# Optimization experiments

Hardware: AMD Instinct MI355X
Metric: run time of the kernel (lower is better)

## Reference

```python
import jax, jax.numpy as jnp
import numpy as np

B, T, D, H = 16, 512, 1024, 16
HD = D // H  # 64
EPS = 1e-5


def _ln(x, g, b):
    m = x.mean(-1, keepdims=True)
    v = ((x - m) ** 2).mean(-1, keepdims=True)
    return (x - m) / jnp.sqrt(v + EPS) * g + b


def setup_inputs() -> dict:
    key = jax.random.key(0)
    ks = jax.random.split(key, 16)
    s = lambda n: 1.0 / np.sqrt(n)
    return {
        "x": jax.random.normal(ks[0], (B, T, D), jnp.float32),
        "ga": jnp.ones((D,), jnp.float32), "ba": jnp.zeros((D,), jnp.float32),
        "Win": jax.random.normal(ks[1], (D, D), jnp.float32) * s(D),
        "bin_": jnp.zeros((D,), jnp.float32),
        "Wk": jax.random.normal(ks[2], (H, D, HD), jnp.float32) * s(D),
        "bk": jnp.zeros((H, HD), jnp.float32),
        "Wq": jax.random.normal(ks[3], (H, D, HD), jnp.float32) * s(D),
        "bq": jnp.zeros((H, HD), jnp.float32),
        "Wv": jax.random.normal(ks[4], (H, D, HD), jnp.float32) * s(D),
        "bv": jnp.zeros((H, HD), jnp.float32),
        "Wout": jax.random.normal(ks[5], (D, D), jnp.float32) * s(D),
        "bout": jnp.zeros((D,), jnp.float32),
        "gf": jnp.ones((D,), jnp.float32), "bf": jnp.zeros((D,), jnp.float32),
        "W1": jax.random.normal(ks[6], (D, 4 * D), jnp.float32) * s(D),
        "b1": jnp.zeros((4 * D,), jnp.float32),
        "W2": jax.random.normal(ks[7], (4 * D, D), jnp.float32) * s(4 * D),
        "b2": jnp.zeros((D,), jnp.float32),
    }


def reference(x, ga, ba, Win, bin_, Wk, bk, Wq, bq, Wv, bv, Wout, bout, gf, bf, W1, b1, W2, b2):
    # --- attention sub-block (pre-norm) ---
    h = _ln(x, ga, ba)
    h = h @ Win + bin_                                   # [B,T,D]
    k = jnp.einsum('btd,hde->bhte', h, Wk) + bk[:, None, :]
    q = jnp.einsum('btd,hde->bhte', h, Wq) + bq[:, None, :]
    v = jnp.einsum('btd,hde->bhte', h, Wv) + bv[:, None, :]
    # NOTE: faithful to source -- scores are K @ Q^T, no 1/sqrt(d) scaling
    wei = jnp.einsum('bhte,bhse->bhts', k, q)            # [B,H,T,T]
    mask = jnp.tril(jnp.ones((T, T), bool))
    wei = jnp.where(mask, wei, -jnp.inf)
    wei = jax.nn.softmax(wei, axis=-1)                   # dropout = eval identity
    o = jnp.einsum('bhts,bhse->bhte', wei, v)            # [B,H,T,HD]
    o = o.transpose(0, 2, 1, 3).reshape(B, T, D)         # concat heads on last dim
    x = o @ Wout + bout + x
    # --- FFN sub-block (pre-norm) ---
    h2 = _ln(x, gf, bf)
    ff = jax.nn.relu(h2 @ W1 + b1) @ W2 + b2
    return ff + x
```

## Files before the change

### kernel.cpp

```cpp
#include <hip/hip_runtime.h>


#define DEV __device__ __forceinline__

typedef unsigned short u16;
typedef __attribute__((ext_vector_type(8))) __bf16 bf16x8;
typedef __attribute__((ext_vector_type(4))) float f32x4;
typedef __attribute__((ext_vector_type(8))) unsigned short u16x8;

typedef __attribute__((address_space(1))) void as1_void;
typedef __attribute__((address_space(3))) void as3_void;

DEV u16 f2b(float f) {
  unsigned u = __float_as_uint(f);
  u = (u + 0x7fffu + ((u >> 16) & 1u)) >> 16;
  return (u16)u;
}
DEV float b2f(u16 h) { return __uint_as_float(((unsigned)h) << 16); }

DEV f32x4 mfma16(bf16x8 a, bf16x8 b, f32x4 c) {
  return __builtin_amdgcn_mfma_f32_16x16x32_bf16(a, b, c, 0, 0, 0);
}

DEV void gload16(const void* g, void* l) {
  __builtin_amdgcn_global_load_lds((as1_void*)(unsigned long long)g,
                                   (as3_void*)(unsigned long long)l,
                                   16u, 0, 0u);
}

#define EPI_BF16 0
#define EPI_RELU 1
#define EPI_RES 2
#define EPI_SPLIT 3
#define EPI_QKFRAG 4
#define EPI_VFRAG 5

template <int BM, int BN, int EPI>
__global__ __launch_bounds__((BM == 256) ? 512 : 256, 2) void gemm256(
    const u16* __restrict__ A, int lda, int kdup, const u16* __restrict__ Bt,
    const float* __restrict__ bias, const float* __restrict__ res,
    void* __restrict__ Cout, void* __restrict__ Cout2, int ldc, int N, int K,
    int ldb, int kdupB) {
  constexpr int THREADS = (BM == 256) ? 512 : 256;
  constexpr int NWAVE = THREADS / 64;
  constexpr int NWN = (BN == 256) ? 4 : 2;
  constexpr int NWM = NWAVE / NWN;
  constexpr int MPW = BM / NWM;
  constexpr int MF = MPW / 16;
  constexpr int LA = BM * 4 / THREADS;
  constexpr int LB = BN * 4 / THREADS;
  constexpr int NWAIT = 2 * (LA + LB);
  constexpr int ASZ = BM * 64;
  constexpr int BSZ = BN * 64;
  constexpr int ATOT = 4 * ASZ;
  __shared__ __align__(1024) char lds[4 * ASZ + 4 * BSZ];

  const int nwg = (int)gridDim.x;
  const int cpx = nwg >> 3;
  int w = (int)blockIdx.x;
  w = (w & 7) * cpx + (w >> 3);
  const int nbn = N / BN;
  const int bn = w % nbn, bm = w / nbn;

  const int tid = threadIdx.x;
  const int wave = tid >> 6, lane = tid & 63;
  const int l15 = lane & 15, l4 = lane >> 4;
  const int wm = wave / NWN;
  const int wn = wave % NWN;
  const int nk = K >> 6;

  const int srow = lane >> 2;
  const int schunk = ((lane & 3) ^ ((srow >> 1) & 3)) << 4;
  const char* Ab = (const char*)A;
  const char* Bb = (const char*)Bt;
  const int arowA = wave * (BM / NWAVE) + srow;
  const int arowB = wave * (BN / NWAVE) + srow;

  auto stageA = [&](int buf, int kh, int kt) {
    const int ktA = (kdup && kt >= kdup) ? kt - kdup : kt;
    const char* s = Ab + (size_t)(bm * BM + arowA) * (size_t)(lda * 2) +
                    ktA * 128 + kh * 64 + schunk;
    char* d = lds + (((buf << 1) | kh) * ASZ) + wave * (LA * 1024);
    gload16(s, d);
    gload16(s + (size_t)16 * (size_t)(lda * 2), d + 1024);
  };
  auto stageB = [&](int buf, int kh, int kt) {
    const int ktB = (kdupB && kt >= kdupB) ? kt - kdupB : kt;
    const char* s = Bb + (size_t)(bn * BN + arowB) * (size_t)(ldb * 2) +
                    ktB * 128 + kh * 64 + schunk;
    char* d = lds + ATOT + (((buf << 1) | kh) * BSZ) + wave * (LB * 1024);
    gload16(s, d);
    if (LB == 2) gload16(s + (size_t)16 * (size_t)(ldb * 2), d + 1024);
  };

  const f32x4 fz = {0.f, 0.f, 0.f, 0.f};
  f32x4 acc[MF][4];
#pragma unroll
  for (int i = 0; i < MF; ++i)
#pragma unroll
    for (int j = 0; j < 4; ++j) acc[i][j] = fz;

  stageA(0, 0, 0);
  stageB(0, 0, 0);
  stageA(0, 1, 0);
  stageB(0, 1, 0);
  {
    const int k1 = (1 < nk) ? 1 : nk - 1;
    stageA(1, 0, k1);
    stageB(1, 0, k1);
  }
  asm volatile("s_waitcnt vmcnt(%0)" ::"i"(NWAIT) : "memory");
  __builtin_amdgcn_s_barrier();

  for (int u = 0; u < nk; ++u) {
    const int cur = u & 1;
    const int kp1 = (u + 1 < nk) ? u + 1 : nk - 1;
    const int kp2 = (u + 2 < nk) ? u + 2 : nk - 1;
#pragma unroll
    for (int kh = 0; kh < 2; ++kh) {
      const char* Ar = lds + (((cur << 1) | kh) * ASZ);
      const char* Br = lds + ATOT + (((cur << 1) | kh) * BSZ);
      bf16x8 bfr[4], af[MF];
#pragma unroll
      for (int ni = 0; ni < 4; ++ni) {
        const int n = wn * 64 + ni * 16 + l15;
        bfr[ni] = *(const bf16x8*)(Br + n * 64 + ((l4 ^ ((n >> 1) & 3)) << 4));
      }
#pragma unroll
      for (int mi = 0; mi < MF; ++mi) {
        const int m = wm * MPW + mi * 16 + l15;
        af[mi] = *(const bf16x8*)(Ar + m * 64 + ((l4 ^ ((m >> 1) & 3)) << 4));
      }
      if (kh == 0) {
        stageA(cur ^ 1, 1, kp1);
        stageB(cur ^ 1, 1, kp1);
      } else {
        stageA(cur, 0, kp2);
        stageB(cur, 0, kp2);
      }
      __builtin_amdgcn_s_setprio(1);
#pragma unroll
      for (int mi = 0; mi < MF; ++mi)
#pragma unroll
        for (int ni = 0; ni < 4; ++ni)
          acc[mi][ni] = mfma16(af[mi], bfr[ni], acc[mi][ni]);
      __builtin_amdgcn_s_setprio(0);
      asm volatile("s_waitcnt lgkmcnt(0)" ::: "memory");
      asm volatile("s_waitcnt vmcnt(%0)" ::"i"(NWAIT) : "memory");
      __builtin_amdgcn_s_barrier();
    }
  }
  asm volatile("s_waitcnt vmcnt(0)" ::: "memory");

#pragma unroll
  for (int mf = 0; mf < MF; ++mf) {
#pragma unroll
    for (int ni = 0; ni < 4; ++ni) {
      const int gn = bn * BN + wn * 64 + ni * 16 + l15;
      const float bia = bias[gn];
#pragma unroll
      for (int r = 0; r < 4; ++r) {
        const int gm = bm * BM + wm * MPW + mf * 16 + l4 * 4 + r;
        float v = acc[mf][ni][r] + bia;
        if (EPI == EPI_BF16) {
          ((u16*)Cout)[(size_t)gm * ldc + gn] = f2b(v);
        } else if (EPI == EPI_RELU) {
          ((u16*)Cout)[(size_t)gm * ldc + gn] = f2b(v > 0.f ? v : 0.f);
        } else if (EPI == EPI_RES) {
          ((float*)Cout)[(size_t)gm * ldc + gn] =
              v + res[(size_t)gm * ldc + gn];
        } else if (EPI == EPI_SPLIT) {
          u16 hi = f2b(v);
          ((u16*)Cout)[(size_t)gm * ldc + gn] = hi;
          ((u16*)Cout)[(size_t)gm * ldc + N + gn] = f2b(v - b2f(hi));
        } else if (EPI == EPI_QKFRAG) {
          const int b = gm >> 9, s = gm & 511;
          const int gs = s >> 4, sr = s & 15;
          const int n = gn & 1023;
          const int h = n >> 6, e = n & 63;
          u16* base = (u16*)((gn >> 10) ? Cout2 : Cout);
          const size_t blk = ((size_t)(b * 16 + h) * 32 + gs) * 4;
          const int idx = ((e >> 3) & 3) * 128 + sr * 8 + (e & 7);
          const u16 hi = f2b(v);
          base[(blk + (e >> 5)) * 512 + idx] = hi;
          base[(blk + 2 + (e >> 5)) * 512 + idx] = f2b(v - b2f(hi));
        } else {
          const int b = gm >> 9, s = gm & 511;
          const int h = gn >> 6, e = gn & 63;
          const size_t blk =
              ((size_t)(b * 16 + h) * 16 + (s >> 5)) * 4 + (e >> 4);
          ((u16*)Cout)[blk * 512 + ((s >> 3) & 3) * 128 + (e & 15) * 8 +
                       (s & 7)] = f2b(v);
        }
      }
    }
  }
}

template <bool SPLIT>
__global__ __launch_bounds__(256) void lnorm(const float* __restrict__ x,
                                             const float* __restrict__ g,
                                             const float* __restrict__ bt,
                                             u16* __restrict__ out) {
  const int row = blockIdx.x, tid = threadIdx.x;
  const int wave = tid >> 6, lane = tid & 63;
  const float4 v = *(const float4*)(x + (size_t)row * 1024 + tid * 4);
  float xv[4] = {v.x, v.y, v.z, v.w};
  float s = xv[0] + xv[1] + xv[2] + xv[3];
  float s2 = xv[0] * xv[0] + xv[1] * xv[1] + xv[2] * xv[2] + xv[3] * xv[3];
  for (int off = 32; off; off >>= 1) {
    s += __shfl_down(s, off);
    s2 += __shfl_down(s2, off);
  }
  __shared__ float red[8];
  if (lane == 0) {
    red[wave] = s;
    red[4 + wave] = s2;
  }
  __syncthreads();
  const float ts = red[0] + red[1] + red[2] + red[3];
  const float ts2 = red[4] + red[5] + red[6] + red[7];
  const float mean = ts * (1.f / 1024.f);
  const float var = ts2 * (1.f / 1024.f) - mean * mean;
  const float rstd = rsqrtf(var + 1e-5f);
#pragma unroll
  for (int j = 0; j < 4; ++j) {
    const int col = tid * 4 + j;
    const float y = (xv[j] - mean) * rstd * g[col] + bt[col];
    const u16 hi = f2b(y);
    if (SPLIT) {
      out[(size_t)row * 2048 + col] = hi;
      out[(size_t)row * 2048 + 1024 + col] = f2b(y - b2f(hi));
    } else {
      out[(size_t)row * 1024 + col] = hi;
    }
  }
}

template <int MODE>
__global__ __launch_bounds__(256) void wtrans(const float* __restrict__ in,
                                              int kstride, long ibs,
                                              u16* __restrict__ out, int ors,
                                              long obs, int Koff) {
  in += (size_t)blockIdx.z * ibs;
  out += (size_t)blockIdx.z * obs;
  const int n0 = blockIdx.x * 64, k0 = blockIdx.y * 64;
  const int tid = threadIdx.x;
  __shared__ float tt[64][65];
  const int r = tid >> 4, c4 = (tid & 15) * 4;
#pragma unroll
  for (int p = 0; p < 4; ++p) {
    const int rr = r + p * 16;
    const float4 vv =
        *(const float4*)(in + (size_t)(k0 + rr) * kstride + n0 + c4);
    tt[rr][c4] = vv.x;
    tt[rr][c4 + 1] = vv.y;
    tt[rr][c4 + 2] = vv.z;
    tt[rr][c4 + 3] = vv.w;
  }
  __syncthreads();
  const int nl = tid >> 2, kc = (tid & 3) * 16;
  u16 hi[16], lo[16];
#pragma unroll
  for (int j = 0; j < 16; ++j) {
    const float w2 = tt[kc + j][nl];
    hi[j] = f2b(w2);
    if (MODE == 2) lo[j] = f2b(w2 - b2f(hi[j]));
  }
  u16* orow = out + (size_t)(n0 + nl) * ors + k0 + kc;
  u16x8 a, b;
#pragma unroll
  for (int j = 0; j < 8; ++j) {
    a[j] = hi[j];
    b[j] = hi[8 + j];
  }
  *(u16x8*)(orow) = a;
  *(u16x8*)(orow + 8) = b;
  if (MODE == 2) {
    *(u16x8*)(orow + 2 * Koff) = a;
    *(u16x8*)(orow + 2 * Koff + 8) = b;
    u16x8 c, d;
#pragma unroll
    for (int j = 0; j < 8; ++j) {
      c[j] = lo[j];
      d[j] = lo[8 + j];
    }
    *(u16x8*)(orow + Koff) = c;
    *(u16x8*)(orow + Koff + 8) = d;
  }
}

__global__ void biascat(const float* __restrict__ bq,
                        const float* __restrict__ bk, float* __restrict__ o) {
  const int i = blockIdx.x * 256 + threadIdx.x;
  o[i] = (i < 1024) ? bq[i] : bk[i - 1024];
}

__global__ void fillconst(float* __restrict__ p, float v, int n) {
  const int i = blockIdx.x * 256 + threadIdx.x;
  if (i < n) p[i] = v;
}

__global__ __launch_bounds__(256) void attn_fwd(const u16* __restrict__ qf,
                                                const u16* __restrict__ kf,
                                                const u16* __restrict__ vf,
                                                u16* __restrict__ o) {
  const int bh = blockIdx.y;
  const int b = bh >> 4, h = bh & 15;
  const int tid = threadIdx.x, wave = tid >> 6, lane = tid & 63;
  const int l15 = lane & 15, l4 = lane >> 4;
  const int g0 = (int)blockIdx.x * 4 + wave;
  __shared__ u16 Pl[4][1024];

  const f32x4 fz = {0.f, 0.f, 0.f, 0.f};
  const u16* qfb = qf + (size_t)bh * 32 * 2048 + lane * 8;
  const u16* vfb = vf + (size_t)bh * 16 * 2048 + lane * 8;

  for (int grp = 0; grp < 2; ++grp) {
    const int gt = grp ? (31 - g0) : g0;
    const int tw = gt * 16;
    const u16* kfb = kf + ((size_t)(bh * 32 + gt) * 4) * 512 + lane * 8;
    const bf16x8 kh0 = *(const bf16x8*)(kfb);
    const bf16x8 kh1 = *(const bf16x8*)(kfb + 512);
    const bf16x8 kl0 = *(const bf16x8*)(kfb + 1024);
    const bf16x8 kl1 = *(const bf16x8*)(kfb + 1536);

    f32x4 oacc[4] = {fz, fz, fz, fz};
    float mrow[4] = {-1e30f, -1e30f, -1e30f, -1e30f};
    float lrow[4] = {0.f, 0.f, 0.f, 0.f};
    const int niter = (tw + 79) >> 6;

    for (int it = 0; it < niter; ++it) {
      const int s0 = it * 64;
      bf16x8 qh[4][2], ql[4][2];
#pragma unroll
      for (int scb = 0; scb < 4; ++scb) {
        const u16* qp = qfb + (size_t)((s0 >> 4) + scb) * 2048;
        qh[scb][0] = *(const bf16x8*)(qp);
        qh[scb][1] = *(const bf16x8*)(qp + 512);
        ql[scb][0] = *(const bf16x8*)(qp + 1024);
        ql[scb][1] = *(const bf16x8*)(qp + 1536);
      }
      bf16x8 vv[2][4];
#pragma unroll
      for (int h2 = 0; h2 < 2; ++h2) {
        const u16* vp = vfb + (size_t)((s0 >> 5) + h2) * 2048;
#pragma unroll
        for (int eF = 0; eF < 4; ++eF)
          vv[h2][eF] = *(const bf16x8*)(vp + eF * 512);
      }
      f32x4 sf[4];
#pragma unroll
      for (int scb = 0; scb < 4; ++scb) {
        f32x4 z = fz;
        z = mfma16(kh0, qh[scb][0], z);
        z = mfma16(kh1, qh[scb][1], z);
        z = mfma16(kh0, ql[scb][0], z);
        z = mfma16(kh1, ql[scb][1], z);
        z = mfma16(kl0, qh[scb][0], z);
        z = mfma16(kl1, qh[scb][1], z);
        sf[scb] = z;
      }
      if (s0 + 63 > tw) {
#pragma unroll
        for (int scb = 0; scb < 4; ++scb)
#pragma unroll
          for (int r = 0; r < 4; ++r) {
            const int s = s0 + scb * 16 + l15, t = tw + l4 * 4 + r;
            if (s > t) sf[scb][r] = -1e30f;
          }
      }
      float scl[4];
#pragma unroll
      for (int r = 0; r < 4; ++r) {
        float v = fmaxf(fmaxf(sf[0][r], sf[1][r]), fmaxf(sf[2][r], sf[3][r]));
        v = fmaxf(v, __shfl_xor(v, 1));
        v = fmaxf(v, __shfl_xor(v, 2));
        v = fmaxf(v, __shfl_xor(v, 4));
        v = fmaxf(v, __shfl_xor(v, 8));
        const float mn = fmaxf(mrow[r], v);
        scl[r] = __expf(mrow[r] - mn);
        mrow[r] = mn;
      }
      float ps[4] = {0.f, 0.f, 0.f, 0.f};
#pragma unroll
      for (int scb = 0; scb < 4; ++scb)
#pragma unroll
        for (int r = 0; r < 4; ++r) {
          const float p = __expf(sf[scb][r] - mrow[r]);
          sf[scb][r] = p;
          ps[r] += p;
        }
#pragma unroll
      for (int r = 0; r < 4; ++r) {
        float v = ps[r];
        v += __shfl_xor(v, 1);
        v += __shfl_xor(v, 2);
        v += __shfl_xor(v, 4);
        v += __shfl_xor(v, 8);
        lrow[r] = lrow[r] * scl[r] + v;
        oacc[0][r] *= scl[r];
        oacc[1][r] *= scl[r];
        oacc[2][r] *= scl[r];
        oacc[3][r] *= scl[r];
      }
#pragma unroll
      for (int scb = 0; scb < 4; ++scb)
#pragma unroll
        for (int r = 0; r < 4; ++r) {
          const int trow = l4 * 4 + r, scol = scb * 16 + l15;
          const int byte = trow * 128 + ((scol * 2) ^ ((trow & 7) << 4));
          *(u16*)((char*)&Pl[wave][0] + byte) = f2b(sf[scb][r]);
        }
#pragma unroll
      for (int h2 = 0; h2 < 2; ++h2) {
        const bf16x8 pf = *(const bf16x8*)((const char*)&Pl[wave][0] +
                                           l15 * 128 +
                                           (((h2 * 4 + l4) ^ (l15 & 7)) << 4));
#pragma unroll
        for (int eF = 0; eF < 4; ++eF)
          oacc[eF] = mfma16(pf, vv[h2][eF], oacc[eF]);
      }
    }
#pragma unroll
    for (int eF = 0; eF < 4; ++eF)
#pragma unroll
      for (int r = 0; r < 4; ++r) {
        const int t = tw + l4 * 4 + r;
        const float val = oacc[eF][r] / lrow[r];
        o[(size_t)(b * 512 + t) * 1024 + h * 64 + eF * 16 + l15] = f2b(val);
      }
  }
}

extern "C" void kernel_launch(void* const* d_in, const int* in_sizes, int n_in,
                              void* d_out, int out_size, void* d_ws,
                              size_t ws_size, hipStream_t stream) {
  const float* x = (const float*)d_in[0];
  const float* ga = (const float*)d_in[1];
  const float* ba = (const float*)d_in[2];
  const float* Win = (const float*)d_in[3];
  const float* bin = (const float*)d_in[4];
  const float* Wk = (const float*)d_in[5];
  const float* bk = (const float*)d_in[6];
  const float* Wq = (const float*)d_in[7];
  const float* bq = (const float*)d_in[8];
  const float* Wv = (const float*)d_in[9];
  const float* bv = (const float*)d_in[10];
  const float* Wout = (const float*)d_in[11];
  const float* bout = (const float*)d_in[12];
  const float* gf = (const float*)d_in[13];
  const float* bf_ = (const float*)d_in[14];
  const float* W1 = (const float*)d_in[15];
  const float* b1 = (const float*)d_in[16];
  const float* W2 = (const float*)d_in[17];
  const float* b2 = (const float*)d_in[18];
  float* out = (float*)d_out;

  char* ws = (char*)d_ws;
  size_t off = 0;
  auto alloc = [&](size_t bytes) {
    char* p = ws + off;
    off += (bytes + 255) & ~(size_t)255;
    return p;
  };
  u16* WinT = (u16*)alloc((size_t)1024 * 1024 * 2);
  u16* WqkT = (u16*)alloc((size_t)2048 * 1024 * 2);
  u16* WvT = (u16*)alloc((size_t)1024 * 1024 * 2);
  u16* WoutT = (u16*)alloc((size_t)1024 * 1024 * 2);
  u16* W1T = (u16*)alloc((size_t)4096 * 1024 * 2);
  u16* W2T = (u16*)alloc((size_t)1024 * 4096 * 2);
  float* bqk = (float*)alloc(2048 * 4);
  char* R1 = alloc((size_t)8192 * 2048 * 2);
  char* R2 = alloc((size_t)8192 * 2048 * 2);
  char* QK = alloc((size_t)2 * 256 * 32 * 4 * 1024);
  const size_t need = off;

  if (need > ws_size) {
    fillconst<<<(out_size + 255) / 256, 256, 0, stream>>>(out, 12345.0f,
                                                          out_size);
    return;
  }

  u16* ln1 = (u16*)R1;
  u16* vfb = (u16*)R1;
  u16* hb = (u16*)R2;
  u16* ob = (u16*)R2;
  u16* ln2 = (u16*)(R2 + (size_t)8192 * 1024 * 2);
  u16* qfb = (u16*)QK;
  u16* kfb = (u16*)(QK + (size_t)256 * 32 * 4 * 1024);
  u16* ffn1 = (u16*)QK;
  float* x2 = out;

  wtrans<0><<<dim3(16, 16, 1), 256, 0, stream>>>(Win, 1024, 0, WinT, 1024, 0,
                                                 0);
  wtrans<0><<<dim3(1, 16, 16), 256, 0, stream>>>(Wq, 64, 65536, WqkT, 1024,
                                                 (long)64 * 1024, 0);
  wtrans<0><<<dim3(1, 16, 16), 256, 0, stream>>>(
      Wk, 64, 65536, WqkT + (size_t)1024 * 1024, 1024, (long)64 * 1024, 0);
  wtrans<0><<<dim3(1, 16, 16), 256, 0, stream>>>(Wv, 64, 65536, WvT, 1024,
                                                 (long)64 * 1024, 0);
  wtrans<0><<<dim3(16, 16, 1), 256, 0, stream>>>(Wout, 1024, 0, WoutT, 1024, 0,
                                                 0);
  wtrans<0><<<dim3(64, 16, 1), 256, 0, stream>>>(W1, 4096, 0, W1T, 1024, 0, 0);
  wtrans<0><<<dim3(16, 64, 1), 256, 0, stream>>>(W2, 1024, 0, W2T, 4096, 0, 0);
  biascat<<<8, 256, 0, stream>>>(bq, bk, bqk);

  lnorm<true><<<8192, 256, 0, stream>>>(x, ga, ba, ln1);
  gemm256<256, 128, EPI_BF16><<<256, 512, 0, stream>>>(
      ln1, 2048, 0, WinT, bin, nullptr, hb, nullptr, 1024, 1024, 2048, 1024,
      16);
  gemm256<256, 256, EPI_QKFRAG><<<256, 512, 0, stream>>>(
      hb, 1024, 0, WqkT, bqk, nullptr, qfb, kfb, 0, 2048, 1024, 1024, 0);
  gemm256<256, 128, EPI_VFRAG><<<256, 512, 0, stream>>>(
      hb, 1024, 0, WvT, bv, nullptr, vfb, nullptr, 0, 1024, 1024, 1024, 0);
  attn_fwd<<<dim3(4, 256), 256, 0, stream>>>(qfb, kfb, vfb, ob);
  gemm256<256, 128, EPI_RES><<<256, 512, 0, stream>>>(
      ob, 1024, 0, WoutT, bout, x, x2, nullptr, 1024, 1024, 1024, 1024, 0);
  lnorm<false><<<8192, 256, 0, stream>>>(x2, gf, bf_, ln2);
  gemm256<256, 256, EPI_RELU><<<512, 512, 0, stream>>>(
      ln2, 1024, 0, W1T, b1, nullptr, ffn1, nullptr, 4096, 4096, 1024, 1024,
      0);
  gemm256<256, 128, EPI_RES><<<256, 512, 0, stream>>>(
      ffn1, 4096, 0, W2T, b2, x2, out, nullptr, 1024, 1024, 4096, 4096, 0);
}
```

Baseline: 390.8 us.

## Drop split-precision LN1 input and fuse Q/K/V projections into one GEMM

The first LayerNorm now writes a single bf16 copy, and the input projection GEMM runs over K=1024 instead of 2048, so the hi/lo split-precision trick on that path is gone. The Q, K and V projections are merged into one GEMM with N=3072 and a combined epilogue that writes Q/K fragments (still hi/lo split) and V fragments. This removes one kernel launch and halves the work of the first projection. In exchange, accuracy drops because the LN1 output is rounded to bf16 once.

Measured after the change: 388.7 us. Within noise of the previous version (-0.5%).

```diff
diff --git a/kernel.cpp b/kernel.cpp
--- a/kernel.cpp
+++ b/kernel.cpp
@@ -31,8 +31,7 @@
 #define EPI_BF16 0
 #define EPI_RELU 1
 #define EPI_RES 2
-#define EPI_SPLIT 3
-#define EPI_QKFRAG 4
+#define EPI_QKV 3
 #define EPI_VFRAG 5
 
 template <int BM, int BN, int EPI>
@@ -169,35 +168,32 @@
         } else if (EPI == EPI_RES) {
           ((float*)Cout)[(size_t)gm * ldc + gn] =
               v + res[(size_t)gm * ldc + gn];
-        } else if (EPI == EPI_SPLIT) {
-          u16 hi = f2b(v);
-          ((u16*)Cout)[(size_t)gm * ldc + gn] = hi;
-          ((u16*)Cout)[(size_t)gm * ldc + N + gn] = f2b(v - b2f(hi));
-        } else if (EPI == EPI_QKFRAG) {
+        } else if (EPI == EPI_QKV) {
           const int b = gm >> 9, s = gm & 511;
-          const int gs = s >> 4, sr = s & 15;
-          const int n = gn & 1023;
-          const int h = n >> 6, e = n & 63;
-          u16* base = (u16*)((gn >> 10) ? Cout2 : Cout);
-          const size_t blk = ((size_t)(b * 16 + h) * 32 + gs) * 4;
-          const int idx = ((e >> 3) & 3) * 128 + sr * 8 + (e & 7);
-          const u16 hi = f2b(v);
-          base[(blk + (e >> 5)) * 512 + idx] = hi;
-          base[(blk + 2 + (e >> 5)) * 512 + idx] = f2b(v - b2f(hi));
-        } else {
-          const int b = gm >> 9, s = gm & 511;
-          const int h = gn >> 6, e = gn & 63;
-          const size_t blk =
-              ((size_t)(b * 16 + h) * 16 + (s >> 5)) * 4 + (e >> 4);
-          ((u16*)Cout)[blk * 512 + ((s >> 3) & 3) * 128 + (e & 15) * 8 +
-                       (s & 7)] = f2b(v);
+          if (gn < 2048) {
+            const int gs = s >> 4, sr = s & 15;
+            const int n = gn & 1023;
+            const int h = n >> 6, e = n & 63;
+            u16* base = (u16*)Cout + ((gn >> 10) ? (size_t)16777216 : 0);
+            const size_t blk = ((size_t)(b * 16 + h) * 32 + gs) * 4;
+            const int idx = ((e >> 3) & 3) * 128 + sr * 8 + (e & 7);
+            const u16 hi = f2b(v);
+            base[(blk + (e >> 5)) * 512 + idx] = hi;
+            base[(blk + 2 + (e >> 5)) * 512 + idx] = f2b(v - b2f(hi));
+          } else {
+            const int n = gn - 2048;
+            const int h = n >> 6, e = n & 63;
+            const size_t blk =
+                ((size_t)(b * 16 + h) * 16 + (s >> 5)) * 4 + (e >> 4);
+            ((u16*)Cout2)[blk * 512 + ((s >> 3) & 3) * 128 + (e & 15) * 8 +
+                          (s & 7)] = f2b(v);
+          }
         }
       }
     }
   }
 }
 
-template <bool SPLIT>
 __global__ __launch_bounds__(256) void lnorm(const float* __restrict__ x,
                                              const float* __restrict__ g,
                                              const float* __restrict__ bt,
@@ -227,21 +223,14 @@
   for (int j = 0; j < 4; ++j) {
     const int col = tid * 4 + j;
     const float y = (xv[j] - mean) * rstd * g[col] + bt[col];
-    const u16 hi = f2b(y);
-    if (SPLIT) {
-      out[(size_t)row * 2048 + col] = hi;
-      out[(size_t)row * 2048 + 1024 + col] = f2b(y - b2f(hi));
-    } else {
-      out[(size_t)row * 1024 + col] = hi;
-    }
-  }
-}
-
-template <int MODE>
+    out[(size_t)row * 1024 + col] = f2b(y);
+  }
+}
+
 __global__ __launch_bounds__(256) void wtrans(const float* __restrict__ in,
                                               int kstride, long ibs,
                                               u16* __restrict__ out, int ors,
-                                              long obs, int Koff) {
+                                              long obs) {
   in += (size_t)blockIdx.z * ibs;
   out += (size_t)blockIdx.z * obs;
   const int n0 = blockIdx.x * 64, k0 = blockIdx.y * 64;
@@ -260,40 +249,22 @@
   }
   __syncthreads();
   const int nl = tid >> 2, kc = (tid & 3) * 16;
-  u16 hi[16], lo[16];
-#pragma unroll
-  for (int j = 0; j < 16; ++j) {
-    const float w2 = tt[kc + j][nl];
-    hi[j] = f2b(w2);
-    if (MODE == 2) lo[j] = f2b(w2 - b2f(hi[j]));
+  u16x8 a, b;
+#pragma unroll
+  for (int j = 0; j < 8; ++j) {
+    a[j] = f2b(tt[kc + j][nl]);
+    b[j] = f2b(tt[kc + 8 + j][nl]);
   }
   u16* orow = out + (size_t)(n0 + nl) * ors + k0 + kc;
-  u16x8 a, b;
-#pragma unroll
-  for (int j = 0; j < 8; ++j) {
-    a[j] = hi[j];
-    b[j] = hi[8 + j];
-  }
   *(u16x8*)(orow) = a;
   *(u16x8*)(orow + 8) = b;
-  if (MODE == 2) {
-    *(u16x8*)(orow + 2 * Koff) = a;
-    *(u16x8*)(orow + 2 * Koff + 8) = b;
-    u16x8 c, d;
-#pragma unroll
-    for (int j = 0; j < 8; ++j) {
-      c[j] = lo[j];
-      d[j] = lo[8 + j];
-    }
-    *(u16x8*)(orow + Koff) = c;
-    *(u16x8*)(orow + Koff + 8) = d;
-  }
-}
-
-__global__ void biascat(const float* __restrict__ bq,
-                        const float* __restrict__ bk, float* __restrict__ o) {
+}
+
+__global__ void biascat3(const float* __restrict__ bq,
+                         const float* __restrict__ bk,
+                         const float* __restrict__ bv, float* __restrict__ o) {
   const int i = blockIdx.x * 256 + threadIdx.x;
-  o[i] = (i < 1024) ? bq[i] : bk[i - 1024];
+  o[i] = (i < 1024) ? bq[i] : (i < 2048 ? bk[i - 1024] : bv[i - 2048]);
 }
 
 __global__ void fillconst(float* __restrict__ p, float v, int n) {
@@ -465,13 +436,12 @@
     return p;
   };
   u16* WinT = (u16*)alloc((size_t)1024 * 1024 * 2);
-  u16* WqkT = (u16*)alloc((size_t)2048 * 1024 * 2);
-  u16* WvT = (u16*)alloc((size_t)1024 * 1024 * 2);
+  u16* WqkvT = (u16*)alloc((size_t)3072 * 1024 * 2);
   u16* WoutT = (u16*)alloc((size_t)1024 * 1024 * 2);
   u16* W1T = (u16*)alloc((size_t)4096 * 1024 * 2);
   u16* W2T = (u16*)alloc((size_t)1024 * 4096 * 2);
-  float* bqk = (float*)alloc(2048 * 4);
-  char* R1 = alloc((size_t)8192 * 2048 * 2);
+  float* bqkv = (float*)alloc(3072 * 4);
+  char* R1 = alloc((size_t)8192 * 1024 * 2);
   char* R2 = alloc((size_t)8192 * 2048 * 2);
   char* QK = alloc((size_t)2 * 256 * 32 * 4 * 1024);
   const size_t need = off;
@@ -492,32 +462,28 @@
   u16* ffn1 = (u16*)QK;
   float* x2 = out;
 
-  wtrans<0><<<dim3(16, 16, 1), 256, 0, stream>>>(Win, 1024, 0, WinT, 1024, 0,
-                                                 0);
-  wtrans<0><<<dim3(1, 16, 16), 256, 0, stream>>>(Wq, 64, 65536, WqkT, 1024,
-                                                 (long)64 * 1024, 0);
-  wtrans<0><<<dim3(1, 16, 16), 256, 0, stream>>>(
-      Wk, 64, 65536, WqkT + (size_t)1024 * 1024, 1024, (long)64 * 1024, 0);
-  wtrans<0><<<dim3(1, 16, 16), 256, 0, stream>>>(Wv, 64, 65536, WvT, 1024,
-                                                 (long)64 * 1024, 0);
-  wtrans<0><<<dim3(16, 16, 1), 256, 0, stream>>>(Wout, 1024, 0, WoutT, 1024, 0,
-                                                 0);
-  wtrans<0><<<dim3(64, 16, 1), 256, 0, stream>>>(W1, 4096, 0, W1T, 1024, 0, 0);
-  wtrans<0><<<dim3(16, 64, 1), 256, 0, stream>>>(W2, 1024, 0, W2T, 4096, 0, 0);
-  biascat<<<8, 256, 0, stream>>>(bq, bk, bqk);
-
-  lnorm<true><<<8192, 256, 0, stream>>>(x, ga, ba, ln1);
+  wtrans<<<dim3(16, 16, 1), 256, 0, stream>>>(Win, 1024, 0, WinT, 1024, 0);
+  wtrans<<<dim3(1, 16, 16), 256, 0, stream>>>(Wq, 64, 65536, WqkvT, 1024,
+                                              (long)64 * 1024);
+  wtrans<<<dim3(1, 16, 16), 256, 0, stream>>>(
+      Wk, 64, 65536, WqkvT + (size_t)1024 * 1024, 1024, (long)64 * 1024);
+  wtrans<<<dim3(1, 16, 16), 256, 0, stream>>>(
+      Wv, 64, 65536, WqkvT + (size_t)2048 * 1024, 1024, (long)64 * 1024);
+  wtrans<<<dim3(16, 16, 1), 256, 0, stream>>>(Wout, 1024, 0, WoutT, 1024, 0);
+  wtrans<<<dim3(64, 16, 1), 256, 0, stream>>>(W1, 4096, 0, W1T, 1024, 0);
+  wtrans<<<dim3(16, 64, 1), 256, 0, stream>>>(W2, 1024, 0, W2T, 4096, 0);
+  biascat3<<<12, 256, 0, stream>>>(bq, bk, bv, bqkv);
+
+  lnorm<<<8192, 256, 0, stream>>>(x, ga, ba, ln1);
   gemm256<256, 128, EPI_BF16><<<256, 512, 0, stream>>>(
-      ln1, 2048, 0, WinT, bin, nullptr, hb, nullptr, 1024, 1024, 2048, 1024,
-      16);
-  gemm256<256, 256, EPI_QKFRAG><<<256, 512, 0, stream>>>(
-      hb, 1024, 0, WqkT, bqk, nullptr, qfb, kfb, 0, 2048, 1024, 1024, 0);
-  gemm256<256, 128, EPI_VFRAG><<<256, 512, 0, stream>>>(
-      hb, 1024, 0, WvT, bv, nullptr, vfb, nullptr, 0, 1024, 1024, 1024, 0);
+      ln1, 1024, 0, WinT, bin, nullptr, hb, nullptr, 1024, 1024, 1024, 1024,
+      0);
+  gemm256<256, 256, EPI_QKV><<<384, 512, 0, stream>>>(
+      hb, 1024, 0, WqkvT, bqkv, nullptr, qfb, vfb, 0, 3072, 1024, 1024, 0);
   attn_fwd<<<dim3(4, 256), 256, 0, stream>>>(qfb, kfb, vfb, ob);
   gemm256<256, 128, EPI_RES><<<256, 512, 0, stream>>>(
       ob, 1024, 0, WoutT, bout, x, x2, nullptr, 1024, 1024, 1024, 1024, 0);
-  lnorm<false><<<8192, 256, 0, stream>>>(x2, gf, bf_, ln2);
+  lnorm<<<8192, 256, 0, stream>>>(x2, gf, bf_, ln2);
   gemm256<256, 256, EPI_RELU><<<512, 512, 0, stream>>>(
       ln2, 1024, 0, W1T, b1, nullptr, ffn1, nullptr, 4096, 4096, 1024, 1024,
       0);
```
